# Optimization experiments

Hardware: AMD Instinct MI355X
Metric: run time of the kernel (lower is better)

Reference implementation:

```python
import jax, jax.numpy as jnp
import numpy as np

B, T, U, D = 2, 512, 48, 512
H, K = 1024, 128  # hidden_channels, num_classes; fc1 in = 2*D = 1024


def setup_inputs() -> dict:
    key = jax.random.key(0)
    ks = jax.random.split(key, 9)
    s = 0.02
    return {
        "img_feature": jax.random.normal(ks[0], (B, T, D), jnp.float32),
        "label_feature": jax.random.normal(ks[1], (B, U, D), jnp.float32),
        "masks": jnp.ones((B, 1, T), jnp.float32),
        "W1": jax.random.normal(ks[2], (H, 2 * D), jnp.float32) * s,
        "b1": jnp.zeros((H,), jnp.float32),
        "W2": jax.random.normal(ks[3], (K, H), jnp.float32) * s,
        "b2": jnp.zeros((K,), jnp.float32),
        "conv_w": jax.random.normal(ks[4], (K, D), jnp.float32) * s,
        "conv_b": jnp.zeros((K,), jnp.float32),
    }


def reference(img_feature, label_feature, masks, W1, b1, W2, b2, conv_w, conv_b):
    # pointwise Conv1d over img features: (B,T,D) -> (B,K,T), masked
    img_seg_score = (jnp.einsum('btd,kd->bkt', img_feature, conv_w)
                     + conv_b[None, :, None]) * masks
    # fc1(cat(label, img)) == label @ Wl^T + img @ Wi^T + b1 (broadcast add),
    # avoiding the O(B*U*T*2D) repeat+cat intermediate.
    d = label_feature.shape[-1]
    Wl, Wi = W1[:, :d], W1[:, d:]
    lab = jnp.einsum('bud,hd->buh', label_feature, Wl)  # (B,U,H)
    img = jnp.einsum('btd,hd->bth', img_feature, Wi)    # (B,T,H)
    h = jnp.tanh(lab[:, :, None, :] + img[:, None, :, :] + b1)  # (B,U,T,H)
    joint = jnp.einsum('buth,kh->butk', h, W2) + b2
    joint_score = jax.nn.log_softmax(joint, axis=-1)
    return (img_seg_score, joint_score)
```

## Files before the change

### kernel.cpp

```cpp
#include <hip/hip_runtime.h>
#include <math.h>

#define BB 2
#define TT 512
#define UU 48
#define DD 512
#define HH 1024
#define KK 128

typedef _Float16 f16x8 __attribute__((ext_vector_type(8)));
typedef __fp16 fp16x2_t __attribute__((ext_vector_type(2)));
typedef float floatx4 __attribute__((ext_vector_type(4)));

__device__ __forceinline__ f16x8 tanh8z(f16x8 z) {
    f16x8 o;
#pragma unroll
    for (int i = 0; i < 8; i += 2) {
        float e0 = __builtin_amdgcn_exp2f((float)z[i]);
        float e1 = __builtin_amdgcn_exp2f((float)z[i + 1]);
        float r0 = __builtin_amdgcn_rcpf(e0 + 1.0f);
        float r1 = __builtin_amdgcn_rcpf(e1 + 1.0f);
        fp16x2_t p = __builtin_amdgcn_cvt_pkrtz(fmaf(-2.0f, r0, 1.0f),
                                                fmaf(-2.0f, r1, 1.0f));
        o[i] = (_Float16)p[0];
        o[i + 1] = (_Float16)p[1];
    }
    return o;
}

__global__ __launch_bounds__(256) void mid_kernel5(
    const float* __restrict__ img, const float* __restrict__ labf,
    const float* __restrict__ W1, const float* __restrict__ W2,
    const float* __restrict__ conv_w,
    const float* __restrict__ b1, const float* __restrict__ conv_b,
    const float* __restrict__ masks,
    _Float16* __restrict__ imgHf, _Float16* __restrict__ labHf,
    _Float16* __restrict__ W2s, float* __restrict__ seg_out) {
    int bid = blockIdx.x, tid = threadIdx.x;
    if (bid >= 624) {
        int base = (bid - 624) * 256 + tid;
#pragma unroll
        for (int i = 0; i < 32; ++i) {
            int o = base + i * 4096;
            int hg = o >> 10, kk2 = (o >> 3) & 127, hl = o & 7;
            W2s[o] = (_Float16)W2[(size_t)kk2 * HH + hg * 8 + hl];
        }
        return;
    }
    __shared__ __align__(16) _Float16 a_s[32][72];
    __shared__ __align__(16) _Float16 w_s[4096];
    const float* Arow;
    const float* Wbase;
    int r0, n0b, wstride, region;
    if (bid < 512) {
        region = 0; Arow = img; Wbase = W1 + 512; wstride = 2 * DD;
        int xcd = bid & 7, j = bid >> 3;
        r0 = (j & 31) * 32; n0b = (xcd * 2 + (j >> 5)) * 64;
    } else if (bid < 560) {
        region = 1; Arow = labf; Wbase = W1; wstride = 2 * DD;
        int i = bid - 512; r0 = (i % 3) * 32; n0b = (i / 3) * 64;
    } else {
        region = 2; Arow = img; Wbase = conv_w; wstride = DD;
        int i = bid - 560; r0 = (i >> 1) * 32; n0b = (i & 1) * 64;
    }
    int lane = tid & 63, wv = tid >> 6;
    int m0 = (wv & 1) * 16, n0w = (wv >> 1) * 32;
    int q = lane >> 4, r = lane & 15;
    int arow = tid >> 3, acol = (tid & 7) * 8;
    int wn = tid >> 2, wk0 = (tid & 3) * 16;
    const float* aptr = &Arow[(size_t)(r0 + arow) * DD + acol];
    const float* wptr = &Wbase[(size_t)(n0b + wn) * wstride + wk0];
    floatx4 acc[2] = {};
    float4 pa0, pa1, pw[4];
    pa0 = *(const float4*)aptr;
    pa1 = *(const float4*)(aptr + 4);
#pragma unroll
    for (int i2 = 0; i2 < 4; ++i2) pw[i2] = *(const float4*)(wptr + i2 * 4);
    for (int c = 0; c < 8; ++c) {
        f16x8 av;
        av[0] = (_Float16)pa0.x; av[1] = (_Float16)pa0.y;
        av[2] = (_Float16)pa0.z; av[3] = (_Float16)pa0.w;
        av[4] = (_Float16)pa1.x; av[5] = (_Float16)pa1.y;
        av[6] = (_Float16)pa1.z; av[7] = (_Float16)pa1.w;
        *(f16x8*)&a_s[arow][acol] = av;
        f16x8 w0, w1;
        w0[0] = (_Float16)pw[0].x; w0[1] = (_Float16)pw[0].y;
        w0[2] = (_Float16)pw[0].z; w0[3] = (_Float16)pw[0].w;
        w0[4] = (_Float16)pw[1].x; w0[5] = (_Float16)pw[1].y;
        w0[6] = (_Float16)pw[1].z; w0[7] = (_Float16)pw[1].w;
        w1[0] = (_Float16)pw[2].x; w1[1] = (_Float16)pw[2].y;
        w1[2] = (_Float16)pw[2].z; w1[3] = (_Float16)pw[2].w;
        w1[4] = (_Float16)pw[3].x; w1[5] = (_Float16)pw[3].y;
        w1[6] = (_Float16)pw[3].z; w1[7] = (_Float16)pw[3].w;
        int kg = wk0 >> 3;
        *(f16x8*)&w_s[((kg + 0) * 64 + wn) * 8] = w0;
        *(f16x8*)&w_s[((kg + 1) * 64 + wn) * 8] = w1;
        __syncthreads();
        if (c < 7) {
            int cb = (c + 1) * 64;
            pa0 = *(const float4*)(aptr + cb);
            pa1 = *(const float4*)(aptr + cb + 4);
#pragma unroll
            for (int i2 = 0; i2 < 4; ++i2)
                pw[i2] = *(const float4*)(wptr + cb + i2 * 4);
        }
#pragma unroll
        for (int kt = 0; kt < 2; ++kt) {
            f16x8 af = *(const f16x8*)&a_s[m0 + r][kt * 32 + q * 8];
#pragma unroll
            for (int nt = 0; nt < 2; ++nt) {
                f16x8 bf = *(const f16x8*)
                    &w_s[((kt * 4 + q) * 64 + n0w + nt * 16 + r) * 8];
                acc[nt] = __builtin_amdgcn_mfma_f32_16x16x32_f16(
                    af, bf, acc[nt], 0, 0, 0);
            }
        }
        __syncthreads();
    }
    const float SC = 2.8853900817779268f;
    if (region == 0) {
#pragma unroll
        for (int nt = 0; nt < 2; ++nt) {
            int n = n0b + n0w + nt * 16 + r;
#pragma unroll
            for (int rr = 0; rr < 4; ++rr)
                imgHf[(size_t)(r0 + m0 + 4 * q + rr) * HH + n] =
                    (_Float16)(acc[nt][rr] * SC);
        }
    } else if (region == 1) {
#pragma unroll
        for (int nt = 0; nt < 2; ++nt) {
            int n = n0b + n0w + nt * 16 + r;
            float bv = b1[n];
#pragma unroll
            for (int rr = 0; rr < 4; ++rr)
                labHf[(size_t)(r0 + m0 + 4 * q + rr) * HH + n] =
                    (_Float16)((acc[nt][rr] + bv) * SC);
        }
    } else {
#pragma unroll
        for (int nt = 0; nt < 2; ++nt) {
            int k = n0b + n0w + nt * 16 + r;
            float bv = conv_b[k];
#pragma unroll
            for (int rr = 0; rr < 4; ++rr) {
                int row = r0 + m0 + 4 * q + rr;
                int b = row >> 9, t = row & 511;
                seg_out[((size_t)b * KK + k) * TT + t] =
                    (acc[nt][rr] + bv) * masks[row];
            }
        }
    }
}

__global__ __launch_bounds__(256) void joint_kernel16(
    const _Float16* __restrict__ imgHf,
    const _Float16* __restrict__ labHf,
    const _Float16* __restrict__ W2s,
    const float* __restrict__ b2,
    float* __restrict__ out) {
    __shared__ __align__(16) _Float16 a_s[64][72];
    __shared__ __align__(16) _Float16 w_s[8192];
    __shared__ __align__(16) _Float16 l_s[64];
    int tid = threadIdx.x, bid = blockIdx.x;
    int lane = tid & 63, wv = tid >> 6;
    int ql = lane >> 4, r = lane & 15;
    int g0 = bid * 64;
    int bu = g0 >> 9;
    int tbase = ((bu >= UU) ? TT : 0) + (g0 & 511);
    int arow = tid >> 2, acol = (tid & 3) * 16;
    const _Float16* ap = imgHf + (size_t)(tbase + arow) * HH + acol;
    const _Float16* wq = W2s + (size_t)tid * 8;
    const _Float16* lp = labHf + (size_t)bu * HH;
    int m0 = wv * 16;
    floatx4 acc[8] = {};
    f16x8 pa0, pa1, pw0, pw1, pw2, pw3, plab;
    pa0 = *(const f16x8*)ap;
    pa1 = *(const f16x8*)(ap + 8);
    pw0 = *(const f16x8*)(wq + 0 * 2048);
    pw1 = *(const f16x8*)(wq + 1 * 2048);
    pw2 = *(const f16x8*)(wq + 2 * 2048);
    pw3 = *(const f16x8*)(wq + 3 * 2048);
    if (tid < 8) plab = *(const f16x8*)(lp + tid * 8);
#pragma unroll 1
    for (int c = 0; c < 16; ++c) {
        *(f16x8*)&a_s[arow][acol] = pa0;
        *(f16x8*)&a_s[arow][acol + 8] = pa1;
        *(f16x8*)&w_s[tid * 8 + 0 * 2048] = pw0;
        *(f16x8*)&w_s[tid * 8 + 1 * 2048] = pw1;
        *(f16x8*)&w_s[tid * 8 + 2 * 2048] = pw2;
        *(f16x8*)&w_s[tid * 8 + 3 * 2048] = pw3;
        if (tid < 8) *(f16x8*)&l_s[tid * 8] = plab;
        __syncthreads();
        if (c < 15) {
            int cb = (c + 1) * 64;
            pa0 = *(const f16x8*)(ap + cb);
            pa1 = *(const f16x8*)(ap + cb + 8);
            const _Float16* wc = wq + (size_t)(c + 1) * 8192;
            pw0 = *(const f16x8*)(wc + 0 * 2048);
            pw1 = *(const f16x8*)(wc + 1 * 2048);
            pw2 = *(const f16x8*)(wc + 2 * 2048);
            pw3 = *(const f16x8*)(wc + 3 * 2048);
            if (tid < 8) plab = *(const f16x8*)(lp + cb + tid * 8);
        }
#pragma unroll
        for (int kt = 0; kt < 2; ++kt) {
            f16x8 af = *(const f16x8*)&a_s[m0 + r][kt * 32 + ql * 8];
            f16x8 lf = *(const f16x8*)&l_s[kt * 32 + ql * 8];
            f16x8 a = tanh8z(af + lf);
#pragma unroll
            for (int nt = 0; nt < 8; ++nt) {
                f16x8 bf = *(const f16x8*)
                    &w_s[((kt * 4 + ql) * 128 + nt * 16 + r) * 8];
                acc[nt] = __builtin_amdgcn_mfma_f32_16x16x32_f16(
                    a, bf, acc[nt], 0, 0, 0);
            }
        }
        __syncthreads();
    }
    float b2v[8];
#pragma unroll
    for (int nt = 0; nt < 8; ++nt) b2v[nt] = b2[nt * 16 + r];
#pragma unroll
    for (int rr = 0; rr < 4; ++rr) {
        float v[8];
        float mx = -INFINITY;
#pragma unroll
        for (int nt = 0; nt < 8; ++nt) {
            v[nt] = acc[nt][rr] + b2v[nt];
            mx = fmaxf(mx, v[nt]);
        }
        mx = fmaxf(mx, __shfl_xor(mx, 1, 16));
        mx = fmaxf(mx, __shfl_xor(mx, 2, 16));
        mx = fmaxf(mx, __shfl_xor(mx, 4, 16));
        mx = fmaxf(mx, __shfl_xor(mx, 8, 16));
        float s = 0.f;
#pragma unroll
        for (int nt = 0; nt < 8; ++nt) s += __expf(v[nt] - mx);
        s += __shfl_xor(s, 1, 16);
        s += __shfl_xor(s, 2, 16);
        s += __shfl_xor(s, 4, 16);
        s += __shfl_xor(s, 8, 16);
        float lse = mx + __logf(s);
        float* orow = out + (size_t)(g0 + m0 + 4 * ql + rr) * KK;
#pragma unroll
        for (int nt = 0; nt < 8; ++nt)
            orow[nt * 16 + r] = v[nt] - lse;
    }
}

extern "C" void kernel_launch(void* const* d_in, const int* in_sizes, int n_in,
                              void* d_out, int out_size, void* d_ws, size_t ws_size,
                              hipStream_t stream) {
    const float* img    = (const float*)d_in[0];
    const float* labf   = (const float*)d_in[1];
    const float* masks  = (const float*)d_in[2];
    const float* W1     = (const float*)d_in[3];
    const float* b1     = (const float*)d_in[4];
    const float* W2     = (const float*)d_in[5];
    const float* b2     = (const float*)d_in[6];
    const float* conv_w = (const float*)d_in[7];
    const float* conv_b = (const float*)d_in[8];
    float* out = (float*)d_out;

    _Float16* base  = (_Float16*)d_ws;
    _Float16* imgHf = base;
    _Float16* labHf = imgHf + 1024 * 1024;
    _Float16* W2s   = labHf + 96 * 1024;

    mid_kernel5<<<640, 256, 0, stream>>>(img, labf, W1, W2, conv_w,
                                         b1, conv_b, masks,
                                         imgHf, labHf, W2s, out);
    joint_kernel16<<<768, 256, 0, stream>>>(imgHf, labHf, W2s, b2,
                                            out + (size_t)BB * KK * TT);
}
```

Measured before the change: 120.6 us.

## Halve joint kernel block to two waves each computing 32 rows

The joint kernel now launches 128 threads per block instead of 256. Each wave handles two 16-row M tiles, so every W2 fragment read from shared memory feeds two MFMAs, and the staging loads are spread over fewer threads with more loads each. This halves LDS reads of B fragments per MFMA and the barrier participants. In exchange each wave holds twice the accumulators and prefetch registers, and each block has fewer waves to hide latency.

Result: slower. 124.9 us (+3.6%).

```diff
diff --git a/kernel.cpp b/kernel.cpp
--- a/kernel.cpp
+++ b/kernel.cpp
@@ -153,7 +153,7 @@
     }
 }
 
-__global__ __launch_bounds__(256) void joint_kernel16(
+__global__ __launch_bounds__(128) void joint_kernel17(
     const _Float16* __restrict__ imgHf,
     const _Float16* __restrict__ labHf,
     const _Float16* __restrict__ W2s,
@@ -163,57 +163,56 @@
     __shared__ __align__(16) _Float16 w_s[8192];
     __shared__ __align__(16) _Float16 l_s[64];
     int tid = threadIdx.x, bid = blockIdx.x;
-    int lane = tid & 63, wv = tid >> 6;
+    int lane = tid & 63, wm = tid >> 6;
     int ql = lane >> 4, r = lane & 15;
     int g0 = bid * 64;
     int bu = g0 >> 9;
     int tbase = ((bu >= UU) ? TT : 0) + (g0 & 511);
-    int arow = tid >> 2, acol = (tid & 3) * 16;
+    int arow = tid >> 1, acol = (tid & 1) * 32;
     const _Float16* ap = imgHf + (size_t)(tbase + arow) * HH + acol;
     const _Float16* wq = W2s + (size_t)tid * 8;
     const _Float16* lp = labHf + (size_t)bu * HH;
-    int m0 = wv * 16;
-    floatx4 acc[8] = {};
-    f16x8 pa0, pa1, pw0, pw1, pw2, pw3, plab;
-    pa0 = *(const f16x8*)ap;
-    pa1 = *(const f16x8*)(ap + 8);
-    pw0 = *(const f16x8*)(wq + 0 * 2048);
-    pw1 = *(const f16x8*)(wq + 1 * 2048);
-    pw2 = *(const f16x8*)(wq + 2 * 2048);
-    pw3 = *(const f16x8*)(wq + 3 * 2048);
+    int m0 = wm * 32;
+    floatx4 acc0[8] = {}, acc1[8] = {};
+    f16x8 pa[4], pw[8], plab;
+#pragma unroll
+    for (int j = 0; j < 4; ++j) pa[j] = *(const f16x8*)(ap + j * 8);
+#pragma unroll
+    for (int j = 0; j < 8; ++j) pw[j] = *(const f16x8*)(wq + j * 1024);
     if (tid < 8) plab = *(const f16x8*)(lp + tid * 8);
 #pragma unroll 1
     for (int c = 0; c < 16; ++c) {
-        *(f16x8*)&a_s[arow][acol] = pa0;
-        *(f16x8*)&a_s[arow][acol + 8] = pa1;
-        *(f16x8*)&w_s[tid * 8 + 0 * 2048] = pw0;
-        *(f16x8*)&w_s[tid * 8 + 1 * 2048] = pw1;
-        *(f16x8*)&w_s[tid * 8 + 2 * 2048] = pw2;
-        *(f16x8*)&w_s[tid * 8 + 3 * 2048] = pw3;
+#pragma unroll
+        for (int j = 0; j < 4; ++j) *(f16x8*)&a_s[arow][acol + j * 8] = pa[j];
+#pragma unroll
+        for (int j = 0; j < 8; ++j) *(f16x8*)&w_s[tid * 8 + j * 1024] = pw[j];
         if (tid < 8) *(f16x8*)&l_s[tid * 8] = plab;
         __syncthreads();
         if (c < 15) {
             int cb = (c + 1) * 64;
-            pa0 = *(const f16x8*)(ap + cb);
-            pa1 = *(const f16x8*)(ap + cb + 8);
+#pragma unroll
+            for (int j = 0; j < 4; ++j)
+                pa[j] = *(const f16x8*)(ap + cb + j * 8);
             const _Float16* wc = wq + (size_t)(c + 1) * 8192;
-            pw0 = *(const f16x8*)(wc + 0 * 2048);
-            pw1 = *(const f16x8*)(wc + 1 * 2048);
-            pw2 = *(const f16x8*)(wc + 2 * 2048);
-            pw3 = *(const f16x8*)(wc + 3 * 2048);
+#pragma unroll
+            for (int j = 0; j < 8; ++j) pw[j] = *(const f16x8*)(wc + j * 1024);
             if (tid < 8) plab = *(const f16x8*)(lp + cb + tid * 8);
         }
 #pragma unroll
         for (int kt = 0; kt < 2; ++kt) {
-            f16x8 af = *(const f16x8*)&a_s[m0 + r][kt * 32 + ql * 8];
             f16x8 lf = *(const f16x8*)&l_s[kt * 32 + ql * 8];
-            f16x8 a = tanh8z(af + lf);
+            f16x8 af0 = *(const f16x8*)&a_s[m0 + r][kt * 32 + ql * 8];
+            f16x8 af1 = *(const f16x8*)&a_s[m0 + 16 + r][kt * 32 + ql * 8];
+            f16x8 a0 = tanh8z(af0 + lf);
+            f16x8 a1 = tanh8z(af1 + lf);
 #pragma unroll
             for (int nt = 0; nt < 8; ++nt) {
                 f16x8 bf = *(const f16x8*)
                     &w_s[((kt * 4 + ql) * 128 + nt * 16 + r) * 8];
-                acc[nt] = __builtin_amdgcn_mfma_f32_16x16x32_f16(
-                    a, bf, acc[nt], 0, 0, 0);
+                acc0[nt] = __builtin_amdgcn_mfma_f32_16x16x32_f16(
+                    a0, bf, acc0[nt], 0, 0, 0);
+                acc1[nt] = __builtin_amdgcn_mfma_f32_16x16x32_f16(
+                    a1, bf, acc1[nt], 0, 0, 0);
             }
         }
         __syncthreads();
@@ -222,30 +221,34 @@
 #pragma unroll
     for (int nt = 0; nt < 8; ++nt) b2v[nt] = b2[nt * 16 + r];
 #pragma unroll
-    for (int rr = 0; rr < 4; ++rr) {
-        float v[8];
-        float mx = -INFINITY;
-#pragma unroll
-        for (int nt = 0; nt < 8; ++nt) {
-            v[nt] = acc[nt][rr] + b2v[nt];
-            mx = fmaxf(mx, v[nt]);
-        }
-        mx = fmaxf(mx, __shfl_xor(mx, 1, 16));
-        mx = fmaxf(mx, __shfl_xor(mx, 2, 16));
-        mx = fmaxf(mx, __shfl_xor(mx, 4, 16));
-        mx = fmaxf(mx, __shfl_xor(mx, 8, 16));
-        float s = 0.f;
-#pragma unroll
-        for (int nt = 0; nt < 8; ++nt) s += __expf(v[nt] - mx);
-        s += __shfl_xor(s, 1, 16);
-        s += __shfl_xor(s, 2, 16);
-        s += __shfl_xor(s, 4, 16);
-        s += __shfl_xor(s, 8, 16);
-        float lse = mx + __logf(s);
-        float* orow = out + (size_t)(g0 + m0 + 4 * ql + rr) * KK;
-#pragma unroll
-        for (int nt = 0; nt < 8; ++nt)
-            orow[nt * 16 + r] = v[nt] - lse;
+    for (int mt = 0; mt < 2; ++mt) {
+#pragma unroll
+        for (int rr = 0; rr < 4; ++rr) {
+            float v[8];
+            float mx = -INFINITY;
+#pragma unroll
+            for (int nt = 0; nt < 8; ++nt) {
+                v[nt] = (mt ? acc1[nt][rr] : acc0[nt][rr]) + b2v[nt];
+                mx = fmaxf(mx, v[nt]);
+            }
+            mx = fmaxf(mx, __shfl_xor(mx, 1, 16));
+            mx = fmaxf(mx, __shfl_xor(mx, 2, 16));
+            mx = fmaxf(mx, __shfl_xor(mx, 4, 16));
+            mx = fmaxf(mx, __shfl_xor(mx, 8, 16));
+            float s = 0.f;
+#pragma unroll
+            for (int nt = 0; nt < 8; ++nt) s += __expf(v[nt] - mx);
+            s += __shfl_xor(s, 1, 16);
+            s += __shfl_xor(s, 2, 16);
+            s += __shfl_xor(s, 4, 16);
+            s += __shfl_xor(s, 8, 16);
+            float lse = mx + __logf(s);
+            float* orow =
+                out + (size_t)(g0 + m0 + mt * 16 + 4 * ql + rr) * KK;
+#pragma unroll
+            for (int nt = 0; nt < 8; ++nt)
+                orow[nt * 16 + r] = v[nt] - lse;
+        }
     }
 }
 
@@ -271,6 +274,6 @@
     mid_kernel5<<<640, 256, 0, stream>>>(img, labf, W1, W2, conv_w,
                                          b1, conv_b, masks,
                                          imgHf, labHf, W2s, out);
-    joint_kernel16<<<768, 256, 0, stream>>>(imgHf, labHf, W2s, b2,
+    joint_kernel17<<<768, 128, 0, stream>>>(imgHf, labHf, W2s, b2,
                                             out + (size_t)BB * KK * TT);
 }
```

## Double-buffer W2 tiles in LDS via direct global-to-LDS loads

Applied to the files above, without the earlier changes.

The joint kernel now copies each W2 chunk straight from global memory into LDS with global_load_lds, instead of staging it through registers. The W2 LDS buffer is double-buffered so chunk c+2 can be loaded while chunk c+1 waits. Register staging of the activation and label tiles is kept, restructured into a prologue plus a second barrier per iteration. This is meant to cut VGPR pressure and store instructions, at the cost of more LDS and an extra barrier. Barrier fences may wait on the outstanding DMA and erase much of the intended overlap.

New measurement: 123.0 us. +2.0%, slower.

```diff
diff --git a/kernel.cpp b/kernel.cpp
--- a/kernel.cpp
+++ b/kernel.cpp
@@ -11,6 +11,9 @@
 typedef _Float16 f16x8 __attribute__((ext_vector_type(8)));
 typedef __fp16 fp16x2_t __attribute__((ext_vector_type(2)));
 typedef float floatx4 __attribute__((ext_vector_type(4)));
+typedef __attribute__((address_space(3))) _Float16 lds_f16;
+typedef __attribute__((address_space(1))) const void g_cvoid;
+typedef __attribute__((address_space(3))) void l_void;
 
 __device__ __forceinline__ f16x8 tanh8z(f16x8 z) {
     f16x8 o;
@@ -153,14 +156,14 @@
     }
 }
 
-__global__ __launch_bounds__(256) void joint_kernel16(
+__global__ __launch_bounds__(256) void joint_kernel18(
     const _Float16* __restrict__ imgHf,
     const _Float16* __restrict__ labHf,
     const _Float16* __restrict__ W2s,
     const float* __restrict__ b2,
     float* __restrict__ out) {
     __shared__ __align__(16) _Float16 a_s[64][72];
-    __shared__ __align__(16) _Float16 w_s[8192];
+    __shared__ __align__(16) _Float16 w_s[2][8192];
     __shared__ __align__(16) _Float16 l_s[64];
     int tid = threadIdx.x, bid = blockIdx.x;
     int lane = tid & 63, wv = tid >> 6;
@@ -170,39 +173,41 @@
     int tbase = ((bu >= UU) ? TT : 0) + (g0 & 511);
     int arow = tid >> 2, acol = (tid & 3) * 16;
     const _Float16* ap = imgHf + (size_t)(tbase + arow) * HH + acol;
-    const _Float16* wq = W2s + (size_t)tid * 8;
     const _Float16* lp = labHf + (size_t)bu * HH;
     int m0 = wv * 16;
     floatx4 acc[8] = {};
-    f16x8 pa0, pa1, pw0, pw1, pw2, pw3, plab;
+
+#define W2DMA(chunk, buf)                                                  \
+    {                                                                      \
+        const _Float16* ws_ = W2s + (size_t)(chunk) * 8192;                \
+        _Pragma("unroll")                                                  \
+        for (int j_ = 0; j_ < 4; ++j_) {                                   \
+            int u_ = tid + j_ * 256;                                       \
+            __builtin_amdgcn_global_load_lds(                              \
+                (g_cvoid*)(ws_ + (size_t)u_ * 8),                          \
+                (l_void*)((lds_f16*)&w_s[buf][(size_t)u_ * 8]), 16, 0, 0); \
+        }                                                                  \
+    }
+
+    f16x8 pa0, pa1, plab;
+    W2DMA(0, 0);
     pa0 = *(const f16x8*)ap;
     pa1 = *(const f16x8*)(ap + 8);
-    pw0 = *(const f16x8*)(wq + 0 * 2048);
-    pw1 = *(const f16x8*)(wq + 1 * 2048);
-    pw2 = *(const f16x8*)(wq + 2 * 2048);
-    pw3 = *(const f16x8*)(wq + 3 * 2048);
     if (tid < 8) plab = *(const f16x8*)(lp + tid * 8);
+    W2DMA(1, 1);
+    *(f16x8*)&a_s[arow][acol] = pa0;
+    *(f16x8*)&a_s[arow][acol + 8] = pa1;
+    if (tid < 8) *(f16x8*)&l_s[tid * 8] = plab;
+    {
+        int cb = 64;
+        pa0 = *(const f16x8*)(ap + cb);
+        pa1 = *(const f16x8*)(ap + cb + 8);
+        if (tid < 8) plab = *(const f16x8*)(lp + cb + tid * 8);
+    }
+    __syncthreads();
 #pragma unroll 1
     for (int c = 0; c < 16; ++c) {
-        *(f16x8*)&a_s[arow][acol] = pa0;
-        *(f16x8*)&a_s[arow][acol + 8] = pa1;
-        *(f16x8*)&w_s[tid * 8 + 0 * 2048] = pw0;
-        *(f16x8*)&w_s[tid * 8 + 1 * 2048] = pw1;
-        *(f16x8*)&w_s[tid * 8 + 2 * 2048] = pw2;
-        *(f16x8*)&w_s[tid * 8 + 3 * 2048] = pw3;
-        if (tid < 8) *(f16x8*)&l_s[tid * 8] = plab;
-        __syncthreads();
-        if (c < 15) {
-            int cb = (c + 1) * 64;
-            pa0 = *(const f16x8*)(ap + cb);
-            pa1 = *(const f16x8*)(ap + cb + 8);
-            const _Float16* wc = wq + (size_t)(c + 1) * 8192;
-            pw0 = *(const f16x8*)(wc + 0 * 2048);
-            pw1 = *(const f16x8*)(wc + 1 * 2048);
-            pw2 = *(const f16x8*)(wc + 2 * 2048);
-            pw3 = *(const f16x8*)(wc + 3 * 2048);
-            if (tid < 8) plab = *(const f16x8*)(lp + cb + tid * 8);
-        }
+        const _Float16* wb = w_s[c & 1];
 #pragma unroll
         for (int kt = 0; kt < 2; ++kt) {
             f16x8 af = *(const f16x8*)&a_s[m0 + r][kt * 32 + ql * 8];
@@ -211,13 +216,27 @@
 #pragma unroll
             for (int nt = 0; nt < 8; ++nt) {
                 f16x8 bf = *(const f16x8*)
-                    &w_s[((kt * 4 + ql) * 128 + nt * 16 + r) * 8];
+                    &wb[((kt * 4 + ql) * 128 + nt * 16 + r) * 8];
                 acc[nt] = __builtin_amdgcn_mfma_f32_16x16x32_f16(
                     a, bf, acc[nt], 0, 0, 0);
             }
         }
         __syncthreads();
-    }
+        if (c < 15) {
+            *(f16x8*)&a_s[arow][acol] = pa0;
+            *(f16x8*)&a_s[arow][acol + 8] = pa1;
+            if (tid < 8) *(f16x8*)&l_s[tid * 8] = plab;
+            if (c < 14) {
+                W2DMA(c + 2, c & 1);
+                int cb = (c + 2) * 64;
+                pa0 = *(const f16x8*)(ap + cb);
+                pa1 = *(const f16x8*)(ap + cb + 8);
+                if (tid < 8) plab = *(const f16x8*)(lp + cb + tid * 8);
+            }
+            __syncthreads();
+        }
+    }
+#undef W2DMA
     float b2v[8];
 #pragma unroll
     for (int nt = 0; nt < 8; ++nt) b2v[nt] = b2[nt * 16 + r];
@@ -271,6 +290,6 @@
     mid_kernel5<<<640, 256, 0, stream>>>(img, labf, W1, W2, conv_w,
                                          b1, conv_b, masks,
                                          imgHf, labHf, W2s, out);
-    joint_kernel16<<<768, 256, 0, stream>>>(imgHf, labHf, W2s, b2,
+    joint_kernel18<<<768, 256, 0, stream>>>(imgHf, labHf, W2s, b2,
                                             out + (size_t)BB * KK * TT);
 }
```
